# Performance work log

Measured on AMD Instinct MI355X. Metric: run time of the kernel, lower is better.

The kernel has to match this reference:

```python
import jax, jax.numpy as jnp
import numpy as np

XLIM = 6.0    # params.max_rdf_dist
DR = 0.05     # params.dr
N_BINS = int(XLIM / DR)  # 120


def setup_inputs() -> dict:
    key = jax.random.key(0)
    k1, k2, k3 = jax.random.split(key, 3)
    T, R, N = 100, 8, 83  # frames, replicas, LiPS atoms
    L = 10.2              # LiPS lattice constant (Angstrom)
    stacked_radii = jax.random.uniform(k1, (T, R, N, 3), dtype=jnp.float32) * L
    # near-cubic LiPS cell with a tiny random skew (non-degenerate lattice)
    cell = jnp.eye(3, dtype=jnp.float32) * L + 0.1 * jax.random.uniform(k2, (3, 3), dtype=jnp.float32)
    gt_rdf = jax.random.uniform(k3, (N_BINS,), dtype=jnp.float32)
    bins = jnp.linspace(1e-6, XLIM, N_BINS + 1).astype(jnp.float32)
    return {"stacked_radii": stacked_radii, "cell": cell, "gt_rdf": gt_rdf, "bins": bins}


def _histogram(d, bins):
    # np.histogram semantics: values outside [bins[0], bins[-1]] dropped,
    # right edge inclusive in the last bin. Zeros (self-distances) fall
    # below bins[0]=1e-6, matching the original's d != 0 filter.
    nb = bins.shape[0] - 1
    idx = jnp.clip(jnp.searchsorted(bins, d, side='right') - 1, 0, nb - 1)
    w = ((d >= bins[0]) & (d <= bins[-1])).astype(jnp.float32)
    return jax.ops.segment_sum(w, idx, num_segments=nb)


def _min_image_dist(x, shifts):
    # x: [T, N, 3]; shifts: [27, 3]. Loop over the 27 fixed shifts to avoid
    # materializing the [T, N, N, 27, 3] tensor the torch code builds.
    diff = x[:, :, None, :] - x[:, None, :, :]            # [T, N, N, 3]
    d2 = jnp.sum((diff - shifts[0]) ** 2, axis=-1)        # [T, N, N]
    for i in range(1, shifts.shape[0]):
        d2 = jnp.minimum(d2, jnp.sum((diff - shifts[i]) ** 2, axis=-1))
    return jnp.sqrt(d2)


def reference(stacked_radii, cell, gt_rdf, bins):
    T, R, N, _ = stacked_radii.shape
    pos = np.arange(-1, 2)  # num_cells = 1 -> 27 periodic images
    combos = jnp.asarray(
        np.stack(np.meshgrid(pos, pos, pos, indexing='xy'), axis=-1).reshape(-1, 3),
        dtype=stacked_radii.dtype)                        # [27, 3]
    shifts = combos @ cell                                # [27, 3]
    volume = jnp.abs(jnp.dot(jnp.cross(cell[0], cell[1]), cell[2]))
    rho = (T * N * N) / volume  # data_shape counted BEFORE zero-filter, as in original
    Z = rho * (4.0 / 3.0) * jnp.pi * (bins[1:] ** 3 - bins[:-1] ** 3)  # [n_bins]

    def rdf_one(x):  # x: [T, N, 3] -> [n_bins]
        d = _min_image_dist(x, shifts)
        return _histogram(d.reshape(-1), bins) / Z

    rdfs = jax.vmap(rdf_one, in_axes=1)(stacked_radii)    # [R, n_bins]
    maes = XLIM * jnp.mean(jnp.abs(rdfs - gt_rdf), axis=-1, keepdims=True)  # [R, 1]
    return rdfs, maes
```

## Files before the change

kernel.cpp:

```cpp
#include <hip/hip_runtime.h>

#define T_FRAMES 100
#define R_REP    8
#define N_ATOMS  83
#define N_BINS   120
#define NWORDS   60
#define NPAIRS   (N_ATOMS * (N_ATOMS - 1) / 2)
#define BLK      512
#define PPT      7
#define SLOTS    T_FRAMES

__device__ __forceinline__ int rowstart(int i) {
    return (i * (165 - i)) >> 1;
}

__global__ __launch_bounds__(BLK) void rdf_hist_kernel(
        const float* __restrict__ radii,
        const float* __restrict__ cell,
        const float* __restrict__ bins,
        unsigned int* __restrict__ partial)
{
#pragma clang fp contract(off)
    __shared__ float4 spos[N_ATOMS];
    __shared__ float4 sfrac[N_ATOMS];
    __shared__ float sbins[N_BINS + 1];
    __shared__ unsigned int shist[N_BINS];

    const int tid = threadIdx.x;
    const int blk = blockIdx.x;
    const int t = blk / R_REP;
    const int r = blk % R_REP;

    float cc[3][3];
#pragma unroll
    for (int c = 0; c < 3; ++c)
#pragma unroll
        for (int d = 0; d < 3; ++d) cc[c][d] = cell[c * 3 + d];
    float rn[3];
#pragma unroll
    for (int c = 0; c < 3; ++c)
        rn[c] = 1.0f / (cc[c][0] * cc[c][0] + cc[c][1] * cc[c][1] + cc[c][2] * cc[c][2]);

    if (tid < N_ATOMS) {
        const float* p = radii + (((size_t)t * R_REP + r) * N_ATOMS + tid) * 3;
        const float x = p[0], y = p[1], z = p[2];
        spos[tid] = make_float4(x, y, z, 0.f);
        sfrac[tid] = make_float4(
            (x * cc[0][0] + y * cc[0][1] + z * cc[0][2]) * rn[0],
            (x * cc[1][0] + y * cc[1][1] + z * cc[1][2]) * rn[1],
            (x * cc[2][0] + y * cc[2][1] + z * cc[2][2]) * rn[2], 0.f);
    }
    if (tid <= N_BINS) sbins[tid] = bins[tid];
    if (tid < N_BINS) shist[tid] = 0u;
    __syncthreads();

    float dx[PPT], dy[PPT], dz[PPT], na[PPT], nb[PPT], nc[PPT];
#pragma unroll
    for (int s = 0; s < PPT; ++s) {
        const int l = tid + s * BLK;
        const int p = (l < NPAIRS) ? l : 0;
        int i = (int)((165.0f - sqrtf((float)(27225 - 8 * p))) * 0.5f);
        if (i < 0) i = 0;
        if (i > N_ATOMS - 2) i = N_ATOMS - 2;
        while (rowstart(i + 1) <= p) ++i;
        while (rowstart(i) > p) --i;
        const int j = p - rowstart(i) + i + 1;
        const float4 pi = spos[i], pj = spos[j];
        const float4 qi = sfrac[i], qj = sfrac[j];
        dx[s] = pi.x - pj.x;
        dy[s] = pi.y - pj.y;
        dz[s] = pi.z - pj.z;
        int axi = (int)floorf(qi.x - qj.x); axi = axi < -1 ? -1 : (axi > 0 ? 0 : axi);
        int ayi = (int)floorf(qi.y - qj.y); ayi = ayi < -1 ? -1 : (ayi > 0 ? 0 : ayi);
        int azi = (int)floorf(qi.z - qj.z); azi = azi < -1 ? -1 : (azi > 0 ? 0 : azi);
        na[s] = (float)axi; nb[s] = (float)ayi; nc[s] = (float)azi;
    }

    float d2m[PPT];
#pragma unroll
    for (int s = 0; s < PPT; ++s) {
        const float Dx = dx[s], Dy = dy[s], Dz = dz[s];
        const float na0 = na[s], na1 = na0 + 1.0f;
        const float nb0 = nb[s], nb1 = nb0 + 1.0f;
        const float nc0 = nc[s], nc1 = nc0 + 1.0f;

        float An[2][3], Bn[2][3], Cn[2][3];
#pragma unroll
        for (int d = 0; d < 3; ++d) {
            An[0][d] = na0 * cc[0][d]; An[1][d] = na1 * cc[0][d];
            Bn[0][d] = nb0 * cc[1][d]; Bn[1][d] = nb1 * cc[1][d];
            Cn[0][d] = nc0 * cc[2][d]; Cn[1][d] = nc1 * cc[2][d];
        }
        float m = 3.4e38f;
#pragma unroll
        for (int ia = 0; ia < 2; ++ia) {
#pragma unroll
            for (int ib = 0; ib < 2; ++ib) {
                const float m0 = An[ia][0] + Bn[ib][0];
                const float m1 = An[ia][1] + Bn[ib][1];
                const float m2 = An[ia][2] + Bn[ib][2];
#pragma unroll
                for (int ic = 0; ic < 2; ++ic) {
                    const float t0 = Dx - (m0 + Cn[ic][0]);
                    const float t1 = Dy - (m1 + Cn[ic][1]);
                    const float t2 = Dz - (m2 + Cn[ic][2]);
                    const float d2 = (t0 * t0 + t1 * t1) + t2 * t2;
                    m = fminf(m, d2);
                }
            }
        }
        d2m[s] = m;
    }

    const float blo = sbins[0];
    const float inv_step = (float)N_BINS / (6.0f - blo);
#pragma unroll
    for (int s = 0; s < PPT; ++s) {
        const int l = tid + s * BLK;
        if (l >= NPAIRS) continue;
        if (d2m[s] > 36.0f) continue;
        const float d = sqrtf(d2m[s]);
        if (d >= blo) {
            int idx = (int)((d - blo) * inv_step);
            if (idx > N_BINS - 1) idx = N_BINS - 1;
            if (idx < 0) idx = 0;
            while (idx > 0 && d < sbins[idx]) --idx;
            while (idx < N_BINS - 1 && d >= sbins[idx + 1]) ++idx;
            atomicAdd(&shist[idx], 2u);
        }
    }
    __syncthreads();

    if (tid < NWORDS) {
        const unsigned int w = shist[2 * tid] | (shist[2 * tid + 1] << 16);
        partial[((size_t)(r * SLOTS + t)) * NWORDS + tid] = w;
    }
}

__global__ __launch_bounds__(256) void finalize_kernel(
        const unsigned int* __restrict__ partial,
        const float* __restrict__ cell,
        const float* __restrict__ bins,
        const float* __restrict__ gt,
        float* __restrict__ out)
{
    __shared__ unsigned int slo[4][NWORDS], shi[4][NWORDS];
    __shared__ float sdiff[N_BINS];
    const int r = blockIdx.x;
    const int tid = threadIdx.x;
    const int h = tid >> 6;
    const int c = tid & 63;

    if (c < NWORDS) {
        const unsigned int* base = partial
            + (size_t)r * SLOTS * NWORDS + (size_t)h * 25 * NWORDS + c;
        unsigned int lo = 0, hi = 0;
#pragma unroll 5
        for (int f = 0; f < 25; ++f) {
            const unsigned int w = base[(size_t)f * NWORDS];
            lo += w & 0xFFFFu;
            hi += w >> 16;
        }
        slo[h][c] = lo;
        shi[h][c] = hi;
    }
    __syncthreads();

    const float c0x = cell[0], c0y = cell[1], c0z = cell[2];
    const float c1x = cell[3], c1y = cell[4], c1z = cell[5];
    const float c2x = cell[6], c2y = cell[7], c2z = cell[8];
    const float crx = c0y * c1z - c0z * c1y;
    const float cry = c0z * c1x - c0x * c1z;
    const float crz = c0x * c1y - c0y * c1x;
    const float vol = fabsf(crx * c2x + cry * c2y + crz * c2z);
    const float rho = (float)(T_FRAMES * N_ATOMS * N_ATOMS) / vol;
    const float coef = (rho * 1.33333337f) * 3.14159274f;

    if (tid < N_BINS) {
        const int w = tid >> 1;
        unsigned int tot = 0;
        if (tid & 1) tot = shi[0][w] + shi[1][w] + shi[2][w] + shi[3][w];
        else         tot = slo[0][w] + slo[1][w] + slo[2][w] + slo[3][w];
        const float b1 = bins[tid], b2 = bins[tid + 1];
        const float Z = coef * (b2 * b2 * b2 - b1 * b1 * b1);
        const float v = (float)tot / Z;
        out[r * N_BINS + tid] = v;
        sdiff[tid] = fabsf(v - gt[tid]);
    }
    __syncthreads();

    if (tid < 64) {
        float s = sdiff[tid] + ((tid < N_BINS - 64) ? sdiff[tid + 64] : 0.0f);
#pragma unroll
        for (int off = 32; off; off >>= 1) s += __shfl_down(s, off, 64);
        if (tid == 0)
            out[R_REP * N_BINS + r] = 6.0f * (s * (1.0f / (float)N_BINS));
    }
}

extern "C" void kernel_launch(void* const* d_in, const int* in_sizes, int n_in,
                              void* d_out, int out_size, void* d_ws, size_t ws_size,
                              hipStream_t stream) {
    const float* radii = (const float*)d_in[0];
    const float* cell  = (const float*)d_in[1];
    const float* gt    = (const float*)d_in[2];
    const float* bins  = (const float*)d_in[3];
    float* out = (float*)d_out;
    unsigned int* part = (unsigned int*)d_ws;

    hipLaunchKernelGGL(rdf_hist_kernel, dim3(T_FRAMES * R_REP), dim3(BLK), 0, stream,
                       radii, cell, bins, part);
    hipLaunchKernelGGL(finalize_kernel, dim3(R_REP), dim3(256), 0, stream,
                       part, cell, bins, gt, out);
}
```

Measured before the change: 27.81 us.

## Fuse finalize into histogram kernel via last-block atomic counter

Removes the separate finalize launch: every histogram block bumps a global atomic counter, and the block that arrives last reduces all replicas' partial histograms, normalizes them and computes the MAE. This removes a kernel launch and the inter-kernel gap. In exchange, the final reduction is serialized onto one block doing 100 loads per wave, and correctness relies on the workspace counter staying consistent (a multiple of the block count) across calls.

```diff
diff --git a/kernel.cpp b/kernel.cpp
--- a/kernel.cpp
+++ b/kernel.cpp
@@ -9,22 +9,29 @@
 #define BLK      512
 #define PPT      7
 #define SLOTS    T_FRAMES
+#define NBLOCKS  (T_FRAMES * R_REP)
 
 __device__ __forceinline__ int rowstart(int i) {
     return (i * (165 - i)) >> 1;
 }
 
-__global__ __launch_bounds__(BLK) void rdf_hist_kernel(
+__global__ __launch_bounds__(BLK) void rdf_fused_kernel(
         const float* __restrict__ radii,
         const float* __restrict__ cell,
         const float* __restrict__ bins,
-        unsigned int* __restrict__ partial)
+        const float* __restrict__ gt,
+        unsigned int* __restrict__ partial,
+        unsigned long long* __restrict__ cnt,
+        float* __restrict__ out)
 {
 #pragma clang fp contract(off)
     __shared__ float4 spos[N_ATOMS];
     __shared__ float4 sfrac[N_ATOMS];
     __shared__ float sbins[N_BINS + 1];
     __shared__ unsigned int shist[N_BINS];
+    __shared__ unsigned int ssum[R_REP][N_BINS];
+    __shared__ float sdiff[R_REP][N_BINS];
+    __shared__ int slast;
 
     const int tid = threadIdx.x;
     const int blk = blockIdx.x;
@@ -133,68 +140,68 @@
 
     if (tid < NWORDS) {
         const unsigned int w = shist[2 * tid] | (shist[2 * tid + 1] << 16);
-        partial[((size_t)(r * SLOTS + t)) * NWORDS + tid] = w;
-    }
-}
-
-__global__ __launch_bounds__(256) void finalize_kernel(
-        const unsigned int* __restrict__ partial,
-        const float* __restrict__ cell,
-        const float* __restrict__ bins,
-        const float* __restrict__ gt,
-        float* __restrict__ out)
-{
-    __shared__ unsigned int slo[4][NWORDS], shi[4][NWORDS];
-    __shared__ float sdiff[N_BINS];
-    const int r = blockIdx.x;
-    const int tid = threadIdx.x;
-    const int h = tid >> 6;
-    const int c = tid & 63;
-
-    if (c < NWORDS) {
-        const unsigned int* base = partial
-            + (size_t)r * SLOTS * NWORDS + (size_t)h * 25 * NWORDS + c;
-        unsigned int lo = 0, hi = 0;
-#pragma unroll 5
-        for (int f = 0; f < 25; ++f) {
-            const unsigned int w = base[(size_t)f * NWORDS];
-            lo += w & 0xFFFFu;
-            hi += w >> 16;
-        }
-        slo[h][c] = lo;
-        shi[h][c] = hi;
-    }
-    __syncthreads();
-
-    const float c0x = cell[0], c0y = cell[1], c0z = cell[2];
-    const float c1x = cell[3], c1y = cell[4], c1z = cell[5];
-    const float c2x = cell[6], c2y = cell[7], c2z = cell[8];
-    const float crx = c0y * c1z - c0z * c1y;
-    const float cry = c0z * c1x - c0x * c1z;
-    const float crz = c0x * c1y - c0y * c1x;
-    const float vol = fabsf(crx * c2x + cry * c2y + crz * c2z);
+        __hip_atomic_store(&partial[((size_t)(r * SLOTS + t)) * NWORDS + tid], w,
+                           __ATOMIC_RELAXED, __HIP_MEMORY_SCOPE_AGENT);
+    }
+    __syncthreads();
+
+    if (tid == 0) {
+        __threadfence();
+        const unsigned long long old = atomicAdd(cnt, 1ull);
+        const int last = ((old % NBLOCKS) == (NBLOCKS - 1));
+        if (last) atomicAdd(cnt, (unsigned long long)0 - (unsigned long long)NBLOCKS);
+        slast = last;
+    }
+    __syncthreads();
+    if (!slast) return;
+    __threadfence();
+
+    {
+        const int w = tid >> 6;
+        const int c = tid & 63;
+        if (c < NWORDS) {
+            const unsigned int* base = partial + (size_t)w * SLOTS * NWORDS + c;
+            unsigned int lo = 0, hi = 0;
+#pragma unroll 10
+            for (int f = 0; f < SLOTS; ++f) {
+                const unsigned int v = __hip_atomic_load(
+                    &base[(size_t)f * NWORDS], __ATOMIC_RELAXED, __HIP_MEMORY_SCOPE_AGENT);
+                lo += v & 0xFFFFu;
+                hi += v >> 16;
+            }
+            ssum[w][2 * c]     = lo;
+            ssum[w][2 * c + 1] = hi;
+        }
+    }
+    __syncthreads();
+
+    const float crx = cc[0][1] * cc[1][2] - cc[0][2] * cc[1][1];
+    const float cry = cc[0][2] * cc[1][0] - cc[0][0] * cc[1][2];
+    const float crz = cc[0][0] * cc[1][1] - cc[0][1] * cc[1][0];
+    const float vol = fabsf(crx * cc[2][0] + cry * cc[2][1] + crz * cc[2][2]);
     const float rho = (float)(T_FRAMES * N_ATOMS * N_ATOMS) / vol;
     const float coef = (rho * 1.33333337f) * 3.14159274f;
 
-    if (tid < N_BINS) {
-        const int w = tid >> 1;
-        unsigned int tot = 0;
-        if (tid & 1) tot = shi[0][w] + shi[1][w] + shi[2][w] + shi[3][w];
-        else         tot = slo[0][w] + slo[1][w] + slo[2][w] + slo[3][w];
-        const float b1 = bins[tid], b2 = bins[tid + 1];
+    for (int e = tid; e < R_REP * N_BINS; e += BLK) {
+        const int rr = e / N_BINS;
+        const int b  = e % N_BINS;
+        const unsigned int tot = ssum[rr][b];
+        const float b1 = sbins[b], b2 = sbins[b + 1];
         const float Z = coef * (b2 * b2 * b2 - b1 * b1 * b1);
         const float v = (float)tot / Z;
-        out[r * N_BINS + tid] = v;
-        sdiff[tid] = fabsf(v - gt[tid]);
-    }
-    __syncthreads();
-
-    if (tid < 64) {
-        float s = sdiff[tid] + ((tid < N_BINS - 64) ? sdiff[tid + 64] : 0.0f);
+        out[e] = v;
+        sdiff[rr][b] = fabsf(v - gt[b]);
+    }
+    __syncthreads();
+
+    {
+        const int w = tid >> 6;
+        const int l = tid & 63;
+        float s = sdiff[w][l] + ((l < N_BINS - 64) ? sdiff[w][l + 64] : 0.0f);
 #pragma unroll
         for (int off = 32; off; off >>= 1) s += __shfl_down(s, off, 64);
-        if (tid == 0)
-            out[R_REP * N_BINS + r] = 6.0f * (s * (1.0f / (float)N_BINS));
+        if (l == 0)
+            out[R_REP * N_BINS + w] = 6.0f * (s * (1.0f / (float)N_BINS));
     }
 }
 
@@ -207,9 +214,9 @@
     const float* bins  = (const float*)d_in[3];
     float* out = (float*)d_out;
     unsigned int* part = (unsigned int*)d_ws;
-
-    hipLaunchKernelGGL(rdf_hist_kernel, dim3(T_FRAMES * R_REP), dim3(BLK), 0, stream,
-                       radii, cell, bins, part);
-    hipLaunchKernelGGL(finalize_kernel, dim3(R_REP), dim3(256), 0, stream,
-                       part, cell, bins, gt, out);
+    unsigned long long* cnt =
+        (unsigned long long*)((char*)d_ws + (size_t)R_REP * SLOTS * NWORDS * 4);
+
+    hipLaunchKernelGGL(rdf_fused_kernel, dim3(NBLOCKS), dim3(BLK), 0, stream,
+                       radii, cell, bins, gt, part, cnt, out);
 }
```

Result: slower. 36.02 us (+29.5%).
